# Kernel optimization log

Hardware: AMD Instinct MI355X
Metric: run time of the kernel (lower is better)

## Reference

```python
import jax, jax.numpy as jnp
import numpy as np

N, R, IN, OUT = 16384, 64, 128, 128


def setup_inputs() -> dict:
    key = jax.random.key(0)
    k1, k2, k3, k4 = jax.random.split(key, 4)
    x = jax.random.normal(k1, (N, IN), dtype=jnp.float32)
    relations = jax.random.randint(k2, (N, 1), 0, R, dtype=jnp.int32)
    # kaiming_uniform_(a=sqrt(5)) on [R, in, out] -> bound = 1/sqrt(fan_in); bias uses same bound
    bound = 1.0 / np.sqrt(IN)
    w = jax.random.uniform(k3, (R, IN, OUT), dtype=jnp.float32, minval=-bound, maxval=bound)
    bias = jax.random.uniform(k4, (R, OUT), dtype=jnp.float32, minval=-bound, maxval=bound)
    return {"x": x, "relations": relations, "w": w, "bias": bias}


def reference(x, relations, w, bias):
    # Faithful math of the torch module: out[i] = x[i] @ w[relations[i,0]] + bias[relations[i,0]]
    # (original computes x.matmul(w[relations]) -> [N,1,N,out] and extracts the diagonal;
    #  this is the direct per-sample grouped GEMM form.)
    rel = relations[:, 0]                       # [N]
    w_sel = jnp.take(w, rel, axis=0)            # [N, in, out]
    out = jnp.einsum('ni,nio->no', x, w_sel)    # [N, out]
    return out + jnp.take(bias, rel, axis=0)
```

## Files before the change

### kernel.cpp

```cpp
#include <hip/hip_runtime.h>

#define N_ROWS 16384
#define R_REL  64
#define IN_D   128
#define OUT_D  128
#define BM     64
#define NS     4
#define TPB    256
#define MAXL   1024

__device__ __forceinline__ float f4c(const float4& v, int i) {
  return i == 0 ? v.x : i == 1 ? v.y : i == 2 ? v.z : v.w;
}

__global__ __launch_bounds__(TPB, 2) void k_fused(const float* __restrict__ x,
                                                  const int* __restrict__ rel,
                                                  const float* __restrict__ w,
                                                  const float* __restrict__ bias,
                                                  float* __restrict__ out) {
  __shared__ __align__(16) float ws_[IN_D * 64];
  __shared__ __align__(16) float xs[BM * IN_D];
  __shared__ int rlist[MAXL];
  __shared__ int wsum[4];
  const int r    = blockIdx.y;
  const int c0   = blockIdx.z * 64;
  const int slab = blockIdx.x;
  const int t    = threadIdx.x;
  const int wid  = t >> 6, lane = t & 63;
  const int tx   = t & 15, ty = t >> 4;

  {
    const float* wr = w + (size_t)r * (IN_D * OUT_D) + c0;
    #pragma unroll
    for (int i = 0; i < 8; ++i) {
      const int id = t + i * 256;
      const int k = id >> 4, c4 = id & 15;
      ((float4*)ws_)[k * 16 + c4] = *(const float4*)(wr + k * OUT_D + c4 * 4);
    }
  }

  const int4* seg = (const int4*)rel + t * 16;
  int c_t = 0;
  #pragma unroll
  for (int i = 0; i < 16; ++i) {
    const int4 v = seg[i];
    c_t += (v.x == r) + (v.y == r) + (v.z == r) + (v.w == r);
  }
  int incl = c_t;
  #pragma unroll
  for (int d = 1; d < 64; d <<= 1) {
    const int u = __shfl_up(incl, d, 64);
    if (lane >= d) incl += u;
  }
  if (lane == 63) wsum[wid] = incl;
  __syncthreads();
  int pos = incl - c_t;
  #pragma unroll
  for (int ww = 0; ww < 4; ++ww) if (ww < wid) pos += wsum[ww];
  const int cntR0 = wsum[0] + wsum[1] + wsum[2] + wsum[3];
  const int cntR = cntR0 < MAXL ? cntR0 : MAXL;
  #pragma unroll
  for (int i = 0; i < 16; ++i) {
    const int4 v = seg[i];
    const int row0 = t * 64 + i * 4;
    if (v.x == r && pos < MAXL) rlist[pos++] = row0;
    if (v.y == r && pos < MAXL) rlist[pos++] = row0 + 1;
    if (v.z == r && pos < MAXL) rlist[pos++] = row0 + 2;
    if (v.w == r && pos < MAXL) rlist[pos++] = row0 + 3;
  }
  __syncthreads();

  for (int tile = slab; tile * BM < cntR; tile += NS) {
    const int t0 = tile * BM;
    const int rows = min(BM, cntR - t0);

    {
      const int row = t & 63;
      const int q = t >> 6;
      if (row < rows) {
        const int g = rlist[t0 + row];
        const float4* src = (const float4*)(x + (size_t)g * IN_D) + q * 8;
        float4* dst = (float4*)xs + row * 32;
        const int sw = row & 7;
        #pragma unroll
        for (int j = 0; j < 8; ++j) dst[(q * 8 + j) ^ sw] = src[j];
      }
    }
    __syncthreads();

    float4 acc[4];
    #pragma unroll
    for (int j = 0; j < 4; ++j) acc[j] = make_float4(0.f, 0.f, 0.f, 0.f);

    const float4* wlds = (const float4*)ws_;
    const float4* xlds = (const float4*)xs;

    #pragma unroll 4
    for (int kc = 0; kc < 32; ++kc) {
      float4 wv[4];
      #pragma unroll
      for (int kk = 0; kk < 4; ++kk) wv[kk] = wlds[(kc * 4 + kk) * 16 + tx];
      float4 xv[4];
      #pragma unroll
      for (int j = 0; j < 4; ++j) {
        const int rm = ty * 4 + j;
        xv[j] = xlds[rm * 32 + (kc ^ (rm & 7))];
      }
      #pragma unroll
      for (int kk = 0; kk < 4; ++kk) {
        #pragma unroll
        for (int j = 0; j < 4; ++j) {
          const float a = f4c(xv[j], kk);
          acc[j].x += a * wv[kk].x;
          acc[j].y += a * wv[kk].y;
          acc[j].z += a * wv[kk].z;
          acc[j].w += a * wv[kk].w;
        }
      }
    }

    const float4 bv = *(const float4*)(bias + (size_t)r * OUT_D + c0 + tx * 4);
    #pragma unroll
    for (int j = 0; j < 4; ++j) {
      const int rm = ty * 4 + j;
      if (rm < rows) {
        const int g = rlist[t0 + rm];
        float4 o;
        o.x = acc[j].x + bv.x;
        o.y = acc[j].y + bv.y;
        o.z = acc[j].z + bv.z;
        o.w = acc[j].w + bv.w;
        *(float4*)(out + (size_t)g * OUT_D + c0 + tx * 4) = o;
      }
    }
    __syncthreads();
  }
}

extern "C" void kernel_launch(void* const* d_in, const int* in_sizes, int n_in,
                              void* d_out, int out_size, void* d_ws, size_t ws_size,
                              hipStream_t stream) {
  const float* x    = (const float*)d_in[0];
  const int*   rel  = (const int*)d_in[1];
  const float* w    = (const float*)d_in[2];
  const float* bias = (const float*)d_in[3];
  float* out = (float*)d_out;

  k_fused<<<dim3(NS, R_REL, 2), TPB, 0, stream>>>(x, rel, w, bias, out);
}
```

Measured before the change: 94.67 us.

## Drop weight LDS staging, read weights from global, shrink row tile

Stops staging the per-relation weight slice in shared memory. Each thread now reads its weight float4s straight from global memory (relying on L1/L2) inside the k loop. The row tile shrinks from 64 to 32 rows with 2 accumulators per thread, the slab count doubles to 8, and launch bounds rise to 6 blocks per CU. The aim is to cut LDS use and register pressure so more blocks run at once and more parallelism covers the rel scan. The cost is repeated global weight reads in the inner loop and a doubled redundant rel count/scan across more blocks.

```diff
diff --git a/kernel.cpp b/kernel.cpp
--- a/kernel.cpp
+++ b/kernel.cpp
@@ -4,8 +4,8 @@
 #define R_REL  64
 #define IN_D   128
 #define OUT_D  128
-#define BM     64
-#define NS     4
+#define BM     32
+#define NSLAB  8
 #define TPB    256
 #define MAXL   1024
 
@@ -13,12 +13,11 @@
   return i == 0 ? v.x : i == 1 ? v.y : i == 2 ? v.z : v.w;
 }
 
-__global__ __launch_bounds__(TPB, 2) void k_fused(const float* __restrict__ x,
+__global__ __launch_bounds__(TPB, 6) void k_fused(const float* __restrict__ x,
                                                   const int* __restrict__ rel,
                                                   const float* __restrict__ w,
                                                   const float* __restrict__ bias,
                                                   float* __restrict__ out) {
-  __shared__ __align__(16) float ws_[IN_D * 64];
   __shared__ __align__(16) float xs[BM * IN_D];
   __shared__ int rlist[MAXL];
   __shared__ int wsum[4];
@@ -28,16 +27,6 @@
   const int t    = threadIdx.x;
   const int wid  = t >> 6, lane = t & 63;
   const int tx   = t & 15, ty = t >> 4;
-
-  {
-    const float* wr = w + (size_t)r * (IN_D * OUT_D) + c0;
-    #pragma unroll
-    for (int i = 0; i < 8; ++i) {
-      const int id = t + i * 256;
-      const int k = id >> 4, c4 = id & 15;
-      ((float4*)ws_)[k * 16 + c4] = *(const float4*)(wr + k * OUT_D + c4 * 4);
-    }
-  }
 
   const int4* seg = (const int4*)rel + t * 16;
   int c_t = 0;
@@ -70,68 +59,66 @@
   }
   __syncthreads();
 
-  for (int tile = slab; tile * BM < cntR; tile += NS) {
+  const float4 bv = *(const float4*)(bias + (size_t)r * OUT_D + c0 + tx * 4);
+  const float* wp = w + (size_t)r * (IN_D * OUT_D) + c0 + tx * 4;
+  const int rm0 = ty * 2, rm1 = ty * 2 + 1;
+  const int sw0 = rm0 & 7, sw1 = rm1 & 7;
+
+  for (int tile = slab; tile * BM < cntR; tile += NSLAB) {
     const int t0 = tile * BM;
     const int rows = min(BM, cntR - t0);
 
     {
-      const int row = t & 63;
-      const int q = t >> 6;
+      const int row = t & 31;
+      const int qb = (t >> 5) * 4;
       if (row < rows) {
         const int g = rlist[t0 + row];
-        const float4* src = (const float4*)(x + (size_t)g * IN_D) + q * 8;
+        const float4* src = (const float4*)(x + (size_t)g * IN_D) + qb;
         float4* dst = (float4*)xs + row * 32;
         const int sw = row & 7;
         #pragma unroll
-        for (int j = 0; j < 8; ++j) dst[(q * 8 + j) ^ sw] = src[j];
+        for (int j = 0; j < 4; ++j) dst[(qb + j) ^ sw] = src[j];
       }
     }
     __syncthreads();
 
-    float4 acc[4];
-    #pragma unroll
-    for (int j = 0; j < 4; ++j) acc[j] = make_float4(0.f, 0.f, 0.f, 0.f);
-
-    const float4* wlds = (const float4*)ws_;
-    const float4* xlds = (const float4*)xs;
+    float4 acc0 = make_float4(0.f, 0.f, 0.f, 0.f);
+    float4 acc1 = make_float4(0.f, 0.f, 0.f, 0.f);
+    const float4* xr0 = (const float4*)xs + rm0 * 32;
+    const float4* xr1 = (const float4*)xs + rm1 * 32;
 
     #pragma unroll 4
     for (int kc = 0; kc < 32; ++kc) {
       float4 wv[4];
       #pragma unroll
-      for (int kk = 0; kk < 4; ++kk) wv[kk] = wlds[(kc * 4 + kk) * 16 + tx];
-      float4 xv[4];
-      #pragma unroll
-      for (int j = 0; j < 4; ++j) {
-        const int rm = ty * 4 + j;
-        xv[j] = xlds[rm * 32 + (kc ^ (rm & 7))];
-      }
+      for (int kk = 0; kk < 4; ++kk)
+        wv[kk] = *(const float4*)(wp + (size_t)(kc * 4 + kk) * OUT_D);
+      const float4 xv0 = xr0[kc ^ sw0];
+      const float4 xv1 = xr1[kc ^ sw1];
       #pragma unroll
       for (int kk = 0; kk < 4; ++kk) {
-        #pragma unroll
-        for (int j = 0; j < 4; ++j) {
-          const float a = f4c(xv[j], kk);
-          acc[j].x += a * wv[kk].x;
-          acc[j].y += a * wv[kk].y;
-          acc[j].z += a * wv[kk].z;
-          acc[j].w += a * wv[kk].w;
-        }
+        const float a0 = f4c(xv0, kk);
+        const float a1 = f4c(xv1, kk);
+        acc0.x += a0 * wv[kk].x;  acc1.x += a1 * wv[kk].x;
+        acc0.y += a0 * wv[kk].y;  acc1.y += a1 * wv[kk].y;
+        acc0.z += a0 * wv[kk].z;  acc1.z += a1 * wv[kk].z;
+        acc0.w += a0 * wv[kk].w;  acc1.w += a1 * wv[kk].w;
       }
     }
 
-    const float4 bv = *(const float4*)(bias + (size_t)r * OUT_D + c0 + tx * 4);
-    #pragma unroll
-    for (int j = 0; j < 4; ++j) {
-      const int rm = ty * 4 + j;
-      if (rm < rows) {
-        const int g = rlist[t0 + rm];
-        float4 o;
-        o.x = acc[j].x + bv.x;
-        o.y = acc[j].y + bv.y;
-        o.z = acc[j].z + bv.z;
-        o.w = acc[j].w + bv.w;
-        *(float4*)(out + (size_t)g * OUT_D + c0 + tx * 4) = o;
-      }
+    if (rm0 < rows) {
+      const int g = rlist[t0 + rm0];
+      float4 o;
+      o.x = acc0.x + bv.x; o.y = acc0.y + bv.y;
+      o.z = acc0.z + bv.z; o.w = acc0.w + bv.w;
+      *(float4*)(out + (size_t)g * OUT_D + c0 + tx * 4) = o;
+    }
+    if (rm1 < rows) {
+      const int g = rlist[t0 + rm1];
+      float4 o;
+      o.x = acc1.x + bv.x; o.y = acc1.y + bv.y;
+      o.z = acc1.z + bv.z; o.w = acc1.w + bv.w;
+      *(float4*)(out + (size_t)g * OUT_D + c0 + tx * 4) = o;
     }
     __syncthreads();
   }
@@ -146,5 +133,5 @@
   const float* bias = (const float*)d_in[3];
   float* out = (float*)d_out;
 
-  k_fused<<<dim3(NS, R_REL, 2), TPB, 0, stream>>>(x, rel, w, bias, out);
+  k_fused<<<dim3(NSLAB, R_REL, 2), TPB, 0, stream>>>(x, rel, w, bias, out);
 }
```

New measurement: 113.7 us. 20.1% more time.
